# Kernel tuning notes

Hardware: AMD Instinct MI355X
Metric: run time of the kernel (lower is better)

Reference implementation:

```python
import jax, jax.numpy as jnp
import numpy as np

NUM_Q_HEADS = 16
NUM_KV_HEADS = 4
HEAD_DIM = 128
HIDDEN = NUM_Q_HEADS * HEAD_DIM
SCALE = 1.0 / HEAD_DIM ** 0.5
NUM_REP = NUM_Q_HEADS // NUM_KV_HEADS
S, B = 2048, 2


def setup_inputs() -> dict:
    key = jax.random.key(0)
    kq, kk, kv = jax.random.split(key, 3)
    query = jax.random.normal(kq, (S, B, NUM_Q_HEADS, HEAD_DIM), dtype=jnp.float32)
    k = jax.random.normal(kk, (S, B, NUM_KV_HEADS, HEAD_DIM), dtype=jnp.float32)
    v = jax.random.normal(kv, (S, B, NUM_KV_HEADS, HEAD_DIM), dtype=jnp.float32)
    return {"query": query, "key": k, "value": v}


def _attn(query, key, value):
    # GQA: repeat kv heads [S,B,Hkv,D] -> [S,B,Hq,D]
    key = jnp.repeat(key, NUM_REP, axis=2)
    value = jnp.repeat(value, NUM_REP, axis=2)
    # fp32 scores, causal mask, softmax (matches torch reference math)
    q32, k32, v32 = query.astype(jnp.float32), key.astype(jnp.float32), value.astype(jnp.float32)
    scores = jnp.einsum('sbhd,tbhd->bhst', q32, k32) * SCALE  # [B,Hq,S,S]
    s = scores.shape[-1]
    causal = jnp.tril(jnp.ones((s, s), dtype=bool))
    scores = jnp.where(causal, scores, -jnp.inf)
    attn = jax.nn.softmax(scores, axis=-1)
    out = jnp.einsum('bhst,tbhd->sbhd', attn, v32)  # [S,B,Hq,D]
    return out.astype(query.dtype).reshape(out.shape[0], out.shape[1], HIDDEN)


def reference(query, key, value) -> jnp.ndarray:
    return _attn(query, key, value)
```

## Files before the change

kernel.cpp:

```cpp
#include <hip/hip_runtime.h>
#include <cstdint>
#include <cstddef>

#define S_LEN 2048
#define BATCH 2
#define HQ    16
#define HKV   4
#define DH    128
#define KVB   64
#define QT0   64
#define KVB0  32
#define VP    40
#define PP    40

typedef float  f4     __attribute__((ext_vector_type(4)));
typedef float  f32x4  __attribute__((ext_vector_type(4)));
typedef float  f32x16 __attribute__((ext_vector_type(16)));
typedef short  short8 __attribute__((ext_vector_type(8)));
typedef unsigned u32x4 __attribute__((ext_vector_type(4)));
typedef __bf16 bf16x8 __attribute__((ext_vector_type(8)));

__device__ __forceinline__ unsigned short f2bf(float x) {
    unsigned u = __builtin_bit_cast(unsigned, x);
    u += 0x7fffu + ((u >> 16) & 1u);
    return (unsigned short)(u >> 16);
}
__device__ __forceinline__ void gld16(const void* g, void* l) {
    __builtin_amdgcn_global_load_lds(
        (const __attribute__((address_space(1))) unsigned int*)g,
        (__attribute__((address_space(3))) unsigned int*)l, 16, 0, 0);
}
__device__ __forceinline__ unsigned cvtpk_bf16(float lo, float hi) {
    unsigned r;
    asm("v_cvt_pk_bf16_f32 %0, %1, %2" : "=v"(r) : "v"(lo), "v"(hi));
    return r;
}

__global__ __launch_bounds__(256)
void prep_k(const float* __restrict__ K, short* __restrict__ out) {
    const int blk = blockIdx.x, bh = blk >> 5, tile = blk & 31, tid = threadIdx.x;
    const int r  = tid >> 2;
    const int s  = tile * 64 + r;
    const int c0 = (tid & 3) * 32;
    const float* src = K + ((size_t)s * (BATCH * HKV) + bh) * DH + c0;
    short* dst = out + ((size_t)bh * S_LEN + s) * DH;
    const int sw = (r & 7) << 3;
    #pragma unroll
    for (int ks = 0; ks < 4; ++ks) {
        f4 a  = ((const f4*)src)[ks * 2];
        f4 b2 = ((const f4*)src)[ks * 2 + 1];
        short8 o;
        #pragma unroll
        for (int j = 0; j < 4; ++j) { o[j] = (short)f2bf(a[j]); o[4 + j] = (short)f2bf(b2[j]); }
        *(short8*)&dst[(c0 + ks * 8) ^ sw] = o;
    }
}

__global__ __launch_bounds__(256)
void prep_v(const float* __restrict__ V, short* __restrict__ out) {
    __shared__ short t[64][136];
    const int blk = blockIdx.x, bh = blk >> 5, tile = blk & 31, tid = threadIdx.x;
    {
        const int r  = tid >> 2;
        const int c0 = (tid & 3) * 32;
        const float* src = V + ((size_t)(tile * 64 + r) * (BATCH * HKV) + bh) * DH + c0;
        #pragma unroll
        for (int m = 0; m < 8; ++m) {
            f4 x = ((const f4*)src)[m];
            #pragma unroll
            for (int j = 0; j < 4; ++j) t[r][c0 + m * 4 + j] = (short)f2bf(x[j]);
        }
    }
    __syncthreads();
    {
        const int d   = tid >> 1;
        const int cc0 = (tid & 1) * 32;
        const int sw  = (d & 7) << 3;
        short* dst = out + (size_t)bh * (S_LEN * DH) + (size_t)tile * (64 * DH) + d * 64 + cc0;
        #pragma unroll
        for (int c8 = 0; c8 < 4; ++c8) {
            const int base = (cc0 + c8 * 8) ^ sw;
            short8 v;
            #pragma unroll
            for (int j = 0; j < 8; ++j) v[j] = t[base + j][d];
            ((short8*)dst)[c8] = v;
        }
    }
}

__global__ __launch_bounds__(512, 1)
void fattn_main(const float* __restrict__ Q, const short* __restrict__ Kb,
                const short* __restrict__ Vb, float* __restrict__ O)
{
    __shared__ short kb[2][2][KVB * DH];
    __shared__ short vb[2][2][DH * KVB];
    __shared__ float xbuf[8][32];

    const int bh  = blockIdx.x;
    const int b   = bh >> 4, h = bh & 15, hkv = h >> 2;
    const int bh2 = b * HKV + hkv;
    const int qx  = 15 - (int)blockIdx.y;
    const int tid = threadIdx.x;
    const int wid = tid >> 6;
    const int lane = tid & 63;
    const int lq  = lane & 31;
    const int hi  = lane >> 5;
    const int half = wid >> 2;
    const int wq0  = qx * 128 + (wid & 3) * 32;
    const int nlo  = qx + 1;

    const float QS = 0.127517244f;
    bf16x8 qf[8];
    {
        const float* qp = Q + ((size_t)(wq0 + lq) * BATCH + b) * (HQ * DH) + h * DH + 8 * hi;
        #pragma unroll
        for (int dstp = 0; dstp < 8; ++dstp) {
            f4 v0 = ((const f4*)(qp + dstp * 16))[0];
            f4 v1 = ((const f4*)(qp + dstp * 16))[1];
            short8 tq;
            #pragma unroll
            for (int j = 0; j < 4; ++j) {
                tq[j]     = (short)f2bf(v0[j] * QS);
                tq[4 + j] = (short)f2bf(v1[j] * QS);
            }
            qf[dstp] = __builtin_bit_cast(bf16x8, tq);
        }
    }

    f32x16 accO[4];
    #pragma unroll
    for (int dblk = 0; dblk < 4; ++dblk)
        #pragma unroll
        for (int r = 0; r < 16; ++r) accO[dblk][r] = 0.f;
    float m = -3.0e38f, dsum = 0.f;

    const char* ksrc = (const char*)(Kb + (size_t)bh2 * S_LEN * DH);
    const char* vsrc = (const char*)(Vb + (size_t)bh2 * S_LEN * DH);

    auto stage = [&](int i) {
        const int tile = (wid >> 2) ? (nlo + i) : i;
        const int isV  = (wid >> 1) & 1;
        const char* src = (isV ? vsrc : ksrc) + (size_t)tile * 16384 + (size_t)(wid & 1) * 8192;
        char* dst = (isV ? (char*)&vb[wid >> 2][i & 1][0] : (char*)&kb[wid >> 2][i & 1][0])
                    + (wid & 1) * 8192;
        #pragma unroll
        for (int j = 0; j < 8; ++j) gld16(src + j * 1024 + lane * 16, dst + j * 1024);
    };

    stage(0);
    __syncthreads();

    for (int i = 0; i < nlo; ++i) {
        if (i + 1 < nlo) stage(i + 1);
        const int t   = half ? (nlo + i) : i;
        const int kv0 = t * 64;
        if (kv0 <= wq0 + 31) {
            const short* kc = kb[half][i & 1];
            const short* vc = vb[half][i & 1];

            f32x16 s0, s1;
            #pragma unroll
            for (int r = 0; r < 16; ++r) { s0[r] = 0.f; s1[r] = 0.f; }
            const int ksw = (lq & 7) << 3;
            const int kr0 = lq * DH, kr1 = (32 + lq) * DH;
            __builtin_amdgcn_s_setprio(1);
            #pragma unroll
            for (int dstp = 0; dstp < 8; ++dstp) {
                const int off = (dstp * 16 + 8 * hi) ^ ksw;
                short8 k0 = *(const short8*)&kc[kr0 + off];
                short8 k1 = *(const short8*)&kc[kr1 + off];
                s0 = __builtin_amdgcn_mfma_f32_32x32x16_bf16(
                    __builtin_bit_cast(bf16x8, k0), qf[dstp], s0, 0, 0, 0);
                s1 = __builtin_amdgcn_mfma_f32_32x32x16_bf16(
                    __builtin_bit_cast(bf16x8, k1), qf[dstp], s1, 0, 0, 0);
            }
            __builtin_amdgcn_s_setprio(0);

            if (kv0 + 63 > wq0) {
                const int q = wq0 + lq;
                const int kvb = kv0 + 4 * hi;
                #pragma unroll
                for (int r = 0; r < 16; ++r) {
                    const int crow = (r & 3) + 8 * (r >> 2);
                    if (kvb + crow > q)      s0[r] = -3.0e38f;
                    if (kvb + 32 + crow > q) s1[r] = -3.0e38f;
                }
            }

            float pm = fmaxf(s0[0], s1[0]);
            #pragma unroll
            for (int r = 1; r < 16; ++r) pm = fmaxf(pm, fmaxf(s0[r], s1[r]));
            pm = fmaxf(pm, __shfl_xor(pm, 32));

            if (!__all(pm <= m + 8.0f)) {
                const float mn = fmaxf(m, pm);
                const float al = __builtin_amdgcn_exp2f(m - mn);
                m = mn;
                if (lane < 32) xbuf[wid][lq] = al;
                #pragma unroll
                for (int g = 0; g < 4; ++g) {
                    f4 av = *(const f4*)&xbuf[wid][g * 8 + 4 * hi];
                    #pragma unroll
                    for (int i2 = 0; i2 < 4; ++i2) {
                        #pragma unroll
                        for (int dblk = 0; dblk < 4; ++dblk)
                            accO[dblk][g * 4 + i2] *= av[i2];
                    }
                }
                dsum *= al;
            }

            float rs = 0.f;
            #pragma unroll
            for (int r = 0; r < 16; ++r) { s0[r] = __builtin_amdgcn_exp2f(s0[r] - m); rs += s0[r]; }
            #pragma unroll
            for (int r = 0; r < 16; ++r) { s1[r] = __builtin_amdgcn_exp2f(s1[r] - m); rs += s1[r]; }
            rs += __shfl_xor(rs, 32);
            dsum += rs;

            bf16x8 pf[4];
            #pragma unroll
            for (int kst = 0; kst < 4; ++kst) {
                const int bo = (kst & 1) * 8;
                float p0, p1, p2, p3, p4, p5, p6, p7;
                if (kst < 2) {
                    p0 = s0[bo + 0]; p1 = s0[bo + 1]; p2 = s0[bo + 2]; p3 = s0[bo + 3];
                    p4 = s0[bo + 4]; p5 = s0[bo + 5]; p6 = s0[bo + 6]; p7 = s0[bo + 7];
                } else {
                    p0 = s1[bo + 0]; p1 = s1[bo + 1]; p2 = s1[bo + 2]; p3 = s1[bo + 3];
                    p4 = s1[bo + 4]; p5 = s1[bo + 5]; p6 = s1[bo + 6]; p7 = s1[bo + 7];
                }
                const unsigned c0 = cvtpk_bf16(p0, p1);
                const unsigned c1 = cvtpk_bf16(p2, p3);
                const unsigned c2 = cvtpk_bf16(p4, p5);
                const unsigned c3 = cvtpk_bf16(p6, p7);
                const unsigned sc0 = (unsigned)__shfl_xor((int)c0, 32);
                const unsigned sc1 = (unsigned)__shfl_xor((int)c1, 32);
                const unsigned sc2 = (unsigned)__shfl_xor((int)c2, 32);
                const unsigned sc3 = (unsigned)__shfl_xor((int)c3, 32);
                u32x4 pw;
                pw[0] = hi ? sc2 : c0;
                pw[1] = hi ? sc3 : c1;
                pw[2] = hi ? c2  : sc0;
                pw[3] = hi ? c3  : sc1;
                pf[kst] = __builtin_bit_cast(bf16x8, pw);
            }

            const int vsw = (lq & 7) << 3;
            __builtin_amdgcn_s_setprio(1);
            #pragma unroll
            for (int kst = 0; kst < 4; ++kst) {
                const int voff = kst * 16 + 8 * hi;
                #pragma unroll
                for (int dblk = 0; dblk < 4; ++dblk) {
                    const int d = dblk * 32 + lq;
                    short8 vv = *(const short8*)&vc[d * KVB + (voff ^ vsw)];
                    accO[dblk] = __builtin_amdgcn_mfma_f32_32x32x16_bf16(
                        pf[kst], __builtin_bit_cast(bf16x8, vv), accO[dblk], 0, 0, 0);
                }
            }
            __builtin_amdgcn_s_setprio(0);
        }
        __syncthreads();
    }

    if (lane < 32) xbuf[wid][lq] = m;
    __syncthreads();
    const float mo = xbuf[wid ^ 4][lq];
    const float ms = fmaxf(m, mo);
    const float aa = __builtin_amdgcn_exp2f(m - ms);
    dsum *= aa;
    __syncthreads();
    if (lane < 32) xbuf[wid][lq] = dsum;
    __syncthreads();
    dsum += xbuf[wid ^ 4][lq];
    __syncthreads();
    if (lane < 32) xbuf[wid][lq] = aa;
    #pragma unroll
    for (int g = 0; g < 4; ++g) {
        f4 av = *(const f4*)&xbuf[wid][g * 8 + 4 * hi];
        #pragma unroll
        for (int i2 = 0; i2 < 4; ++i2) {
            #pragma unroll
            for (int dblk = 0; dblk < 4; ++dblk)
                accO[dblk][g * 4 + i2] *= av[i2];
        }
    }
    __syncthreads();
    float* mb = (float*)&kb[0][0][0];
    if (half) {
        float* slot = mb + (size_t)(wid & 3) * 4096;
        #pragma unroll
        for (int dblk = 0; dblk < 4; ++dblk)
            #pragma unroll
            for (int r2 = 0; r2 < 4; ++r2) {
                f4 v;
                #pragma unroll
                for (int j = 0; j < 4; ++j) v[j] = accO[dblk][r2 * 4 + j];
                *(f4*)&slot[(dblk * 4 + r2) * 256 + lane * 4] = v;
            }
    }
    __syncthreads();
    if (!half) {
        float* slot = mb + (size_t)(wid & 3) * 4096;
        #pragma unroll
        for (int dblk = 0; dblk < 4; ++dblk)
            #pragma unroll
            for (int r2 = 0; r2 < 4; ++r2) {
                f4 v = *(const f4*)&slot[(dblk * 4 + r2) * 256 + lane * 4];
                #pragma unroll
                for (int j = 0; j < 4; ++j) accO[dblk][r2 * 4 + j] += v[j];
            }
        if (lane < 32) xbuf[wid][lq] = dsum;
        #pragma unroll
        for (int g = 0; g < 4; ++g) {
            f4 dv = *(const f4*)&xbuf[wid][g * 8 + 4 * hi];
            #pragma unroll
            for (int i2 = 0; i2 < 4; ++i2) {
                const float inv = 1.0f / dv[i2];
                const int row = wq0 + g * 8 + i2 + 4 * hi;
                float* op = O + ((size_t)row * BATCH + b) * (HQ * DH) + h * DH + lq;
                #pragma unroll
                for (int dblk = 0; dblk < 4; ++dblk)
                    op[dblk * 32] = accO[dblk][g * 4 + i2] * inv;
            }
        }
    }
}

__global__ __launch_bounds__(256)
void fattn_fallback(const float* __restrict__ Q, const float* __restrict__ K,
                    const float* __restrict__ V, float* __restrict__ O)
{
    __shared__ short kbuf[KVB0 * DH];
    __shared__ short vbuf[DH * VP];
    __shared__ short pbuf[4][16 * PP];

    const int bh  = blockIdx.y;
    const int b   = bh >> 4, h = bh & 15, hkv = h >> 2;
    const int q0  = blockIdx.x * QT0;
    const int tid = threadIdx.x;
    const int wid = tid >> 6;
    const int lane = tid & 63;
    const int lr  = lane & 15;
    const int kb2 = lane >> 4;
    const int qr  = q0 + wid * 16;

    const float QS = 0.127517244f;
    bf16x8 qf[4];
    {
        const float* qp = Q + ((size_t)(qr + lr) * BATCH + b) * (HQ * DH) + h * DH + kb2 * 8;
        #pragma unroll
        for (int ks = 0; ks < 4; ++ks) {
            f4 v0 = ((const f4*)(qp + ks * 32))[0];
            f4 v1 = ((const f4*)(qp + ks * 32))[1];
            short8 tq;
            #pragma unroll
            for (int j = 0; j < 4; ++j) {
                tq[j]     = (short)f2bf(v0[j] * QS);
                tq[4 + j] = (short)f2bf(v1[j] * QS);
            }
            qf[ks] = __builtin_bit_cast(bf16x8, tq);
        }
    }

    float mr[4], ls[4];
    f32x4 accO[8];
    #pragma unroll
    for (int r = 0; r < 4; ++r) { mr[r] = -3.0e38f; ls[r] = 0.0f; }
    #pragma unroll
    for (int d = 0; d < 8; ++d) accO[d] = (f32x4){0.f, 0.f, 0.f, 0.f};

    const int sr  = tid >> 3, sc = tid & 7;
    const int vr2 = (tid >> 4) * 2, vc8 = tid & 15;
    const int ntiles = q0 / KVB0 + 2;

    for (int t = 0; t < ntiles; ++t) {
        const int kv0 = t * KVB0;
        {
            const float* kp = K + ((size_t)(kv0 + sr) * BATCH + b) * (HKV * DH) + hkv * DH + sc * 16;
            f4 a0 = ((const f4*)kp)[0];
            f4 a1 = ((const f4*)kp)[1];
            f4 a2 = ((const f4*)kp)[2];
            f4 a3 = ((const f4*)kp)[3];
            short8 s0v, s1v;
            #pragma unroll
            for (int j = 0; j < 4; ++j) {
                s0v[j] = (short)f2bf(a0[j]); s0v[4 + j] = (short)f2bf(a1[j]);
                s1v[j] = (short)f2bf(a2[j]); s1v[4 + j] = (short)f2bf(a3[j]);
            }
            const int sw = (sr & 7) << 3;
            *(short8*)&kbuf[sr * DH + ((sc * 16) ^ sw)]     = s0v;
            *(short8*)&kbuf[sr * DH + ((sc * 16 + 8) ^ sw)] = s1v;
        }
        {
            const float* vp0 = V + ((size_t)(kv0 + vr2) * BATCH + b) * (HKV * DH) + hkv * DH + vc8 * 8;
            const float* vp1 = vp0 + (size_t)BATCH * HKV * DH;
            f4 b0 = ((const f4*)vp0)[0];
            f4 b1 = ((const f4*)vp0)[1];
            f4 c0 = ((const f4*)vp1)[0];
            f4 c1 = ((const f4*)vp1)[1];
            float va[8]  = {b0[0], b0[1], b0[2], b0[3], b1[0], b1[1], b1[2], b1[3]};
            float vbv[8] = {c0[0], c0[1], c0[2], c0[3], c1[0], c1[1], c1[2], c1[3]};
            #pragma unroll
            for (int j = 0; j < 8; ++j) {
                const int d = vc8 * 8 + j;
                unsigned pk = (unsigned)f2bf(va[j]) | ((unsigned)f2bf(vbv[j]) << 16);
                const int rsw = (((vr2 >> 3) ^ ((d >> 3) & 3)) << 3) + (vr2 & 7);
                *(unsigned*)&vbuf[d * VP + rsw] = pk;
            }
        }
        __syncthreads();

        f32x4 sf[2];
        sf[0] = (f32x4){0.f, 0.f, 0.f, 0.f};
        sf[1] = (f32x4){0.f, 0.f, 0.f, 0.f};
        #pragma unroll
        for (int cb = 0; cb < 2; ++cb) {
            const int krow = cb * 16 + lr;
            const int sw = (krow & 7) << 3;
            #pragma unroll
            for (int ks = 0; ks < 4; ++ks) {
                short8 kkf = *(const short8*)&kbuf[krow * DH + ((ks * 32 + kb2 * 8) ^ sw)];
                sf[cb] = __builtin_amdgcn_mfma_f32_16x16x32_bf16(
                    qf[ks], __builtin_bit_cast(bf16x8, kkf), sf[cb], 0, 0, 0);
            }
        }
        if (kv0 + KVB0 - 1 > qr) {
            #pragma unroll
            for (int cb = 0; cb < 2; ++cb) {
                const int col = kv0 + cb * 16 + lr;
                #pragma unroll
                for (int r = 0; r < 4; ++r)
                    if (col > qr + kb2 * 4 + r) sf[cb][r] = -3.0e38f;
            }
        }
        float al[4];
        #pragma unroll
        for (int r = 0; r < 4; ++r) {
            float rm = fmaxf(sf[0][r], sf[1][r]);
            rm = fmaxf(rm, __shfl_xor(rm, 1));
            rm = fmaxf(rm, __shfl_xor(rm, 2));
            rm = fmaxf(rm, __shfl_xor(rm, 4));
            rm = fmaxf(rm, __shfl_xor(rm, 8));
            const float mn = fmaxf(mr[r], rm);
            al[r] = exp2f(mr[r] - mn);
            mr[r] = mn;
            const unsigned short pk0 = f2bf(exp2f(sf[0][r] - mn));
            const unsigned short pk1 = f2bf(exp2f(sf[1][r] - mn));
            pbuf[wid][(kb2 * 4 + r) * PP + lr]      = (short)pk0;
            pbuf[wid][(kb2 * 4 + r) * PP + 16 + lr] = (short)pk1;
            float ps = __builtin_bit_cast(float, (unsigned)pk0 << 16)
                     + __builtin_bit_cast(float, (unsigned)pk1 << 16);
            ps += __shfl_xor(ps, 1);
            ps += __shfl_xor(ps, 2);
            ps += __shfl_xor(ps, 4);
            ps += __shfl_xor(ps, 8);
            ls[r] = ls[r] * al[r] + ps;
        }
        #pragma unroll
        for (int d = 0; d < 8; ++d) {
            #pragma unroll
            for (int r = 0; r < 4; ++r) accO[d][r] *= al[r];
        }
        const short8 pA = *(const short8*)&pbuf[wid][lr * PP + kb2 * 8];
        #pragma unroll
        for (int db = 0; db < 8; ++db) {
            const int d = db * 16 + lr;
            const int rc = ((kb2 ^ ((d >> 3) & 3)) << 3);
            short8 vv = *(const short8*)&vbuf[d * VP + rc];
            accO[db] = __builtin_amdgcn_mfma_f32_16x16x32_bf16(
                __builtin_bit_cast(bf16x8, pA), __builtin_bit_cast(bf16x8, vv), accO[db], 0, 0, 0);
        }
        __syncthreads();
    }

    #pragma unroll
    for (int r = 0; r < 4; ++r) ls[r] = 1.0f / ls[r];
    #pragma unroll
    for (int db = 0; db < 8; ++db) {
        #pragma unroll
        for (int r = 0; r < 4; ++r) {
            const int row = qr + kb2 * 4 + r;
            O[((size_t)row * BATCH + b) * (HQ * DH) + h * DH + db * 16 + lr] = accO[db][r] * ls[r];
        }
    }
}

extern "C" void kernel_launch(void* const* d_in, const int* in_sizes, int n_in,
                              void* d_out, int out_size, void* d_ws, size_t ws_size,
                              hipStream_t stream)
{
    (void)in_sizes; (void)n_in; (void)out_size;
    const float* Q = (const float*)d_in[0];
    const float* K = (const float*)d_in[1];
    const float* V = (const float*)d_in[2];
    float* O = (float*)d_out;

    const size_t kv_elems = (size_t)BATCH * HKV * S_LEN * DH;
    const size_t need = kv_elems * 2 * sizeof(short);
    if (ws_size >= need) {
        short* Kb = (short*)d_ws;
        short* Vb = Kb + kv_elems;
        prep_k<<<dim3(BATCH * HKV * (S_LEN / 64)), dim3(256), 0, stream>>>(K, Kb);
        prep_v<<<dim3(BATCH * HKV * (S_LEN / 64)), dim3(256), 0, stream>>>(V, Vb);
        dim3 grid(BATCH * HQ, 16);
        fattn_main<<<grid, dim3(512), 0, stream>>>(Q, Kb, Vb, O);
    } else {
        dim3 grid(S_LEN / QT0, BATCH * HQ);
        fattn_fallback<<<grid, dim3(256), 0, stream>>>(Q, K, V, O);
    }
}
```

Before: 74.88 us.

## Split causal KV loop across four wave groups with 32-wide tiles

fattn_main grows from 8 to 16 waves per block. Four query-row groups each walk an interleaved stream of 32-wide KV tiles instead of two halves walking 64-wide tiles. Each step then runs half the MFMAs per wave, with its own masking and softmax. prep_v is rewritten to emit the V layout these 32-column tiles need. A multi-stage LDS reduction merges the four partial softmax states and outputs, which adds more barriers and a launch-bounds setting that may constrain registers.

```diff
diff --git a/kernel.cpp b/kernel.cpp
--- a/kernel.cpp
+++ b/kernel.cpp
@@ -7,7 +7,6 @@
 #define HQ    16
 #define HKV   4
 #define DH    128
-#define KVB   64
 #define QT0   64
 #define KVB0  32
 #define VP    40
@@ -59,11 +58,11 @@
 __global__ __launch_bounds__(256)
 void prep_v(const float* __restrict__ V, short* __restrict__ out) {
     __shared__ short t[64][136];
-    const int blk = blockIdx.x, bh = blk >> 5, tile = blk & 31, tid = threadIdx.x;
+    const int blk = blockIdx.x, bh = blk >> 5, tile64 = blk & 31, tid = threadIdx.x;
     {
         const int r  = tid >> 2;
         const int c0 = (tid & 3) * 32;
-        const float* src = V + ((size_t)(tile * 64 + r) * (BATCH * HKV) + bh) * DH + c0;
+        const float* src = V + ((size_t)(tile64 * 64 + r) * (BATCH * HKV) + bh) * DH + c0;
         #pragma unroll
         for (int m = 0; m < 8; ++m) {
             f4 x = ((const f4*)src)[m];
@@ -74,27 +73,32 @@
     __syncthreads();
     {
         const int d   = tid >> 1;
-        const int cc0 = (tid & 1) * 32;
-        const int sw  = (d & 7) << 3;
-        short* dst = out + (size_t)bh * (S_LEN * DH) + (size_t)tile * (64 * DH) + d * 64 + cc0;
-        #pragma unroll
-        for (int c8 = 0; c8 < 4; ++c8) {
-            const int base = (cc0 + c8 * 8) ^ sw;
-            short8 v;
-            #pragma unroll
-            for (int j = 0; j < 8; ++j) v[j] = t[base + j][d];
-            ((short8*)dst)[c8] = v;
-        }
-    }
-}
-
-__global__ __launch_bounds__(512, 1)
+        const int h16 = tid & 1;
+        const int rr  = d >> 1;
+        const int sw  = (rr & 7) << 3;
+        short* base = out + (size_t)bh * (S_LEN * DH);
+        #pragma unroll
+        for (int a = 0; a < 2; ++a) {
+            short* dst = base + (size_t)(2 * tile64 + a) * 4096 + rr * 64;
+            #pragma unroll
+            for (int g = 0; g < 2; ++g) {
+                const int kv0 = h16 * 16 + g * 8;
+                const int cb  = (d & 1) * 32 + kv0;
+                short8 v;
+                #pragma unroll
+                for (int j = 0; j < 8; ++j) v[j] = t[a * 32 + kv0 + j][d];
+                *(short8*)&dst[cb ^ sw] = v;
+            }
+        }
+    }
+}
+
+__global__ __launch_bounds__(1024, 4)
 void fattn_main(const float* __restrict__ Q, const short* __restrict__ Kb,
                 const short* __restrict__ Vb, float* __restrict__ O)
 {
-    __shared__ short kb[2][2][KVB * DH];
-    __shared__ short vb[2][2][DH * KVB];
-    __shared__ float xbuf[8][32];
+    __shared__ short kvs[4][2][2][4096];
+    __shared__ float xbuf[16][32];
 
     const int bh  = blockIdx.x;
     const int b   = bh >> 4, h = bh & 15, hkv = h >> 2;
@@ -105,9 +109,10 @@
     const int lane = tid & 63;
     const int lq  = lane & 31;
     const int hi  = lane >> 5;
-    const int half = wid >> 2;
-    const int wq0  = qx * 128 + (wid & 3) * 32;
-    const int nlo  = qx + 1;
+    const int rw  = wid & 3;
+    const int qt  = wid >> 2;
+    const int wq0 = qx * 128 + rw * 32;
+    const int nit = qx + 1;
 
     const float QS = 0.127517244f;
     bf16x8 qf[8];
@@ -138,58 +143,51 @@
     const char* vsrc = (const char*)(Vb + (size_t)bh2 * S_LEN * DH);
 
     auto stage = [&](int i) {
-        const int tile = (wid >> 2) ? (nlo + i) : i;
-        const int isV  = (wid >> 1) & 1;
-        const char* src = (isV ? vsrc : ksrc) + (size_t)tile * 16384 + (size_t)(wid & 1) * 8192;
-        char* dst = (isV ? (char*)&vb[wid >> 2][i & 1][0] : (char*)&kb[wid >> 2][i & 1][0])
-                    + (wid & 1) * 8192;
-        #pragma unroll
-        for (int j = 0; j < 8; ++j) gld16(src + j * 1024 + lane * 16, dst + j * 1024);
+        const int qs  = wid >> 2;
+        const int isV = (wid >> 1) & 1;
+        const int t   = 4 * i + qs;
+        const char* src = (isV ? vsrc : ksrc) + (size_t)t * 8192 + (size_t)(wid & 1) * 4096;
+        char* dst = (char*)&kvs[qs][i & 1][isV][0] + (wid & 1) * 4096;
+        #pragma unroll
+        for (int j = 0; j < 4; ++j) gld16(src + j * 1024 + lane * 16, dst + j * 1024);
     };
 
     stage(0);
     __syncthreads();
 
-    for (int i = 0; i < nlo; ++i) {
-        if (i + 1 < nlo) stage(i + 1);
-        const int t   = half ? (nlo + i) : i;
-        const int kv0 = t * 64;
+    for (int i = 0; i < nit; ++i) {
+        if (i + 1 < nit) stage(i + 1);
+        const int kv0 = (4 * i + qt) * 32;
         if (kv0 <= wq0 + 31) {
-            const short* kc = kb[half][i & 1];
-            const short* vc = vb[half][i & 1];
-
-            f32x16 s0, s1;
-            #pragma unroll
-            for (int r = 0; r < 16; ++r) { s0[r] = 0.f; s1[r] = 0.f; }
+            const short* kc = &kvs[qt][i & 1][0][0];
+            const short* vc = &kvs[qt][i & 1][1][0];
+
+            f32x16 s0;
+            #pragma unroll
+            for (int r = 0; r < 16; ++r) s0[r] = 0.f;
             const int ksw = (lq & 7) << 3;
-            const int kr0 = lq * DH, kr1 = (32 + lq) * DH;
             __builtin_amdgcn_s_setprio(1);
             #pragma unroll
             for (int dstp = 0; dstp < 8; ++dstp) {
-                const int off = (dstp * 16 + 8 * hi) ^ ksw;
-                short8 k0 = *(const short8*)&kc[kr0 + off];
-                short8 k1 = *(const short8*)&kc[kr1 + off];
+                short8 k0 = *(const short8*)&kc[lq * DH + ((dstp * 16 + 8 * hi) ^ ksw)];
                 s0 = __builtin_amdgcn_mfma_f32_32x32x16_bf16(
                     __builtin_bit_cast(bf16x8, k0), qf[dstp], s0, 0, 0, 0);
-                s1 = __builtin_amdgcn_mfma_f32_32x32x16_bf16(
-                    __builtin_bit_cast(bf16x8, k1), qf[dstp], s1, 0, 0, 0);
             }
             __builtin_amdgcn_s_setprio(0);
 
-            if (kv0 + 63 > wq0) {
+            if (kv0 + 31 > wq0) {
                 const int q = wq0 + lq;
                 const int kvb = kv0 + 4 * hi;
                 #pragma unroll
                 for (int r = 0; r < 16; ++r) {
                     const int crow = (r & 3) + 8 * (r >> 2);
-                    if (kvb + crow > q)      s0[r] = -3.0e38f;
-                    if (kvb + 32 + crow > q) s1[r] = -3.0e38f;
+                    if (kvb + crow > q) s0[r] = -3.0e38f;
                 }
             }
 
-            float pm = fmaxf(s0[0], s1[0]);
-            #pragma unroll
-            for (int r = 1; r < 16; ++r) pm = fmaxf(pm, fmaxf(s0[r], s1[r]));
+            float pm = s0[0];
+            #pragma unroll
+            for (int r = 1; r < 16; ++r) pm = fmaxf(pm, s0[r]);
             pm = fmaxf(pm, __shfl_xor(pm, 32));
 
             if (!__all(pm <= m + 8.0f)) {
@@ -213,27 +211,17 @@
             float rs = 0.f;
             #pragma unroll
             for (int r = 0; r < 16; ++r) { s0[r] = __builtin_amdgcn_exp2f(s0[r] - m); rs += s0[r]; }
-            #pragma unroll
-            for (int r = 0; r < 16; ++r) { s1[r] = __builtin_amdgcn_exp2f(s1[r] - m); rs += s1[r]; }
             rs += __shfl_xor(rs, 32);
             dsum += rs;
 
-            bf16x8 pf[4];
-            #pragma unroll
-            for (int kst = 0; kst < 4; ++kst) {
-                const int bo = (kst & 1) * 8;
-                float p0, p1, p2, p3, p4, p5, p6, p7;
-                if (kst < 2) {
-                    p0 = s0[bo + 0]; p1 = s0[bo + 1]; p2 = s0[bo + 2]; p3 = s0[bo + 3];
-                    p4 = s0[bo + 4]; p5 = s0[bo + 5]; p6 = s0[bo + 6]; p7 = s0[bo + 7];
-                } else {
-                    p0 = s1[bo + 0]; p1 = s1[bo + 1]; p2 = s1[bo + 2]; p3 = s1[bo + 3];
-                    p4 = s1[bo + 4]; p5 = s1[bo + 5]; p6 = s1[bo + 6]; p7 = s1[bo + 7];
-                }
-                const unsigned c0 = cvtpk_bf16(p0, p1);
-                const unsigned c1 = cvtpk_bf16(p2, p3);
-                const unsigned c2 = cvtpk_bf16(p4, p5);
-                const unsigned c3 = cvtpk_bf16(p6, p7);
+            bf16x8 pf[2];
+            #pragma unroll
+            for (int kst = 0; kst < 2; ++kst) {
+                const int bo = kst * 8;
+                const unsigned c0 = cvtpk_bf16(s0[bo + 0], s0[bo + 1]);
+                const unsigned c1 = cvtpk_bf16(s0[bo + 2], s0[bo + 3]);
+                const unsigned c2 = cvtpk_bf16(s0[bo + 4], s0[bo + 5]);
+                const unsigned c3 = cvtpk_bf16(s0[bo + 6], s0[bo + 7]);
                 const unsigned sc0 = (unsigned)__shfl_xor((int)c0, 32);
                 const unsigned sc1 = (unsigned)__shfl_xor((int)c1, 32);
                 const unsigned sc2 = (unsigned)__shfl_xor((int)c2, 32);
@@ -246,15 +234,15 @@
                 pf[kst] = __builtin_bit_cast(bf16x8, pw);
             }
 
-            const int vsw = (lq & 7) << 3;
             __builtin_amdgcn_s_setprio(1);
             #pragma unroll
-            for (int kst = 0; kst < 4; ++kst) {
-                const int voff = kst * 16 + 8 * hi;
+            for (int kst = 0; kst < 2; ++kst) {
                 #pragma unroll
                 for (int dblk = 0; dblk < 4; ++dblk) {
-                    const int d = dblk * 32 + lq;
-                    short8 vv = *(const short8*)&vc[d * KVB + (voff ^ vsw)];
+                    const int d  = dblk * 32 + lq;
+                    const int rr = d >> 1;
+                    const int col = (d & 1) * 32 + kst * 16 + 8 * hi;
+                    short8 vv = *(const short8*)&vc[rr * 64 + (col ^ ((rr & 7) << 3))];
                     accO[dblk] = __builtin_amdgcn_mfma_f32_32x32x16_bf16(
                         pf[kst], __builtin_bit_cast(bf16x8, vv), accO[dblk], 0, 0, 0);
                 }
@@ -266,14 +254,14 @@
 
     if (lane < 32) xbuf[wid][lq] = m;
     __syncthreads();
-    const float mo = xbuf[wid ^ 4][lq];
-    const float ms = fmaxf(m, mo);
-    const float aa = __builtin_amdgcn_exp2f(m - ms);
+    const float m4 = fmaxf(fmaxf(xbuf[rw][lq], xbuf[rw + 4][lq]),
+                           fmaxf(xbuf[rw + 8][lq], xbuf[rw + 12][lq]));
+    const float aa = __builtin_amdgcn_exp2f(m - m4);
     dsum *= aa;
     __syncthreads();
     if (lane < 32) xbuf[wid][lq] = dsum;
     __syncthreads();
-    dsum += xbuf[wid ^ 4][lq];
+    const float dtot = xbuf[rw][lq] + xbuf[rw + 4][lq] + xbuf[rw + 8][lq] + xbuf[rw + 12][lq];
     __syncthreads();
     if (lane < 32) xbuf[wid][lq] = aa;
     #pragma unroll
@@ -287,9 +275,9 @@
         }
     }
     __syncthreads();
-    float* mb = (float*)&kb[0][0][0];
-    if (half) {
-        float* slot = mb + (size_t)(wid & 3) * 4096;
+    float* mb = (float*)&kvs[0][0][0][0];
+    if (qt == 1 || qt == 3) {
+        float* slot = mb + (size_t)(rw + ((qt == 3) ? 4 : 0)) * 4096;
         #pragma unroll
         for (int dblk = 0; dblk < 4; ++dblk)
             #pragma unroll
@@ -301,8 +289,8 @@
             }
     }
     __syncthreads();
-    if (!half) {
-        float* slot = mb + (size_t)(wid & 3) * 4096;
+    if (qt == 0 || qt == 2) {
+        float* slot = mb + (size_t)(rw + ((qt == 2) ? 4 : 0)) * 4096;
         #pragma unroll
         for (int dblk = 0; dblk < 4; ++dblk)
             #pragma unroll
@@ -311,7 +299,33 @@
                 #pragma unroll
                 for (int j = 0; j < 4; ++j) accO[dblk][r2 * 4 + j] += v[j];
             }
-        if (lane < 32) xbuf[wid][lq] = dsum;
+    }
+    __syncthreads();
+    if (qt == 2) {
+        float* slot = mb + (size_t)rw * 4096;
+        #pragma unroll
+        for (int dblk = 0; dblk < 4; ++dblk)
+            #pragma unroll
+            for (int r2 = 0; r2 < 4; ++r2) {
+                f4 v;
+                #pragma unroll
+                for (int j = 0; j < 4; ++j) v[j] = accO[dblk][r2 * 4 + j];
+                *(f4*)&slot[(dblk * 4 + r2) * 256 + lane * 4] = v;
+            }
+    }
+    __syncthreads();
+    if (lane < 32) xbuf[wid][lq] = dtot;
+    __syncthreads();
+    if (qt == 0) {
+        float* slot = mb + (size_t)rw * 4096;
+        #pragma unroll
+        for (int dblk = 0; dblk < 4; ++dblk)
+            #pragma unroll
+            for (int r2 = 0; r2 < 4; ++r2) {
+                f4 v = *(const f4*)&slot[(dblk * 4 + r2) * 256 + lane * 4];
+                #pragma unroll
+                for (int j = 0; j < 4; ++j) accO[dblk][r2 * 4 + j] += v[j];
+            }
         #pragma unroll
         for (int g = 0; g < 4; ++g) {
             f4 dv = *(const f4*)&xbuf[wid][g * 8 + 4 * hi];
@@ -505,7 +519,7 @@
         prep_k<<<dim3(BATCH * HKV * (S_LEN / 64)), dim3(256), 0, stream>>>(K, Kb);
         prep_v<<<dim3(BATCH * HKV * (S_LEN / 64)), dim3(256), 0, stream>>>(V, Vb);
         dim3 grid(BATCH * HQ, 16);
-        fattn_main<<<grid, dim3(512), 0, stream>>>(Q, Kb, Vb, O);
+        fattn_main<<<grid, dim3(1024), 0, stream>>>(Q, Kb, Vb, O);
     } else {
         dim3 grid(S_LEN / QT0, BATCH * HQ);
         fattn_fallback<<<grid, dim3(256), 0, stream>>>(Q, K, V, O);
```

Measured after the change: 139.5 us. 1.86x slower.

## Split KV halves into separate workgroups and merge partial outputs in a second kernel

Applied to the files above, without the earlier changes.

Replaces the single 512-thread block that processes two KV halves internally with 256-thread blocks, one per KV half, doubling the grid and allowing two blocks per CU. Each block writes an unnormalized partial output plus its row max and sum to workspace. A new merge kernel combines the two halves with log-sum-exp rescaling. The aim is better occupancy and load balance, at the cost of an extra fp32 output round trip through global memory and another kernel launch. The old kernel is kept as a fallback when the workspace is too small.

```diff
diff --git a/kernel.cpp b/kernel.cpp
--- a/kernel.cpp
+++ b/kernel.cpp
@@ -88,26 +88,28 @@
     }
 }
 
-__global__ __launch_bounds__(512, 1)
-void fattn_main(const float* __restrict__ Q, const short* __restrict__ Kb,
-                const short* __restrict__ Vb, float* __restrict__ O)
+__global__ __launch_bounds__(256, 2)
+void fattn_half(const float* __restrict__ Q, const short* __restrict__ Kb,
+                const short* __restrict__ Vb, float* __restrict__ Olo,
+                float* __restrict__ Whi, float* __restrict__ ml)
 {
-    __shared__ short kb[2][2][KVB * DH];
-    __shared__ short vb[2][2][DH * KVB];
-    __shared__ float xbuf[8][32];
+    __shared__ short kb[2][KVB * DH];
+    __shared__ short vb[2][DH * KVB];
+    __shared__ float xbuf[4][32];
 
     const int bh  = blockIdx.x;
     const int b   = bh >> 4, h = bh & 15, hkv = h >> 2;
     const int bh2 = b * HKV + hkv;
-    const int qx  = 15 - (int)blockIdx.y;
+    const int y   = blockIdx.y;
+    const int qx  = 15 - (y >> 1);
+    const int half = y & 1;
     const int tid = threadIdx.x;
     const int wid = tid >> 6;
     const int lane = tid & 63;
     const int lq  = lane & 31;
     const int hi  = lane >> 5;
-    const int half = wid >> 2;
-    const int wq0  = qx * 128 + (wid & 3) * 32;
-    const int nlo  = qx + 1;
+    const int wq0 = qx * 128 + wid * 32;
+    const int nlo = qx + 1;
 
     const float QS = 0.127517244f;
     bf16x8 qf[8];
@@ -138,11 +140,10 @@
     const char* vsrc = (const char*)(Vb + (size_t)bh2 * S_LEN * DH);
 
     auto stage = [&](int i) {
-        const int tile = (wid >> 2) ? (nlo + i) : i;
-        const int isV  = (wid >> 1) & 1;
-        const char* src = (isV ? vsrc : ksrc) + (size_t)tile * 16384 + (size_t)(wid & 1) * 8192;
-        char* dst = (isV ? (char*)&vb[wid >> 2][i & 1][0] : (char*)&kb[wid >> 2][i & 1][0])
-                    + (wid & 1) * 8192;
+        const int t   = half ? (nlo + i) : i;
+        const int isV = (wid >> 1) & 1;
+        const char* src = (isV ? vsrc : ksrc) + (size_t)t * 16384 + (size_t)(wid & 1) * 8192;
+        char* dst = (isV ? (char*)&vb[i & 1][0] : (char*)&kb[i & 1][0]) + (wid & 1) * 8192;
         #pragma unroll
         for (int j = 0; j < 8; ++j) gld16(src + j * 1024 + lane * 16, dst + j * 1024);
     };
@@ -155,8 +156,8 @@
         const int t   = half ? (nlo + i) : i;
         const int kv0 = t * 64;
         if (kv0 <= wq0 + 31) {
-            const short* kc = kb[half][i & 1];
-            const short* vc = vb[half][i & 1];
+            const short* kc = kb[i & 1];
+            const short* vc = vb[i & 1];
 
             f32x16 s0, s1;
             #pragma unroll
@@ -264,6 +265,229 @@
         __syncthreads();
     }
 
+    const int part = (qx * 32 + bh) * 2 + half;
+    if (lane < 32) {
+        ml[(size_t)part * 256 + wid * 32 + lq]       = m;
+        ml[(size_t)part * 256 + 128 + wid * 32 + lq] = dsum;
+    }
+    float* Od = half ? Whi : Olo;
+    #pragma unroll
+    for (int g = 0; g < 4; ++g) {
+        #pragma unroll
+        for (int i2 = 0; i2 < 4; ++i2) {
+            const int row = wq0 + g * 8 + i2 + 4 * hi;
+            float* op = Od + ((size_t)row * BATCH + b) * (HQ * DH) + h * DH + lq;
+            #pragma unroll
+            for (int dblk = 0; dblk < 4; ++dblk)
+                op[dblk * 32] = accO[dblk][g * 4 + i2];
+        }
+    }
+}
+
+__global__ __launch_bounds__(256)
+void merge_halves(float* __restrict__ O, const float* __restrict__ Whi,
+                  const float* __restrict__ ml)
+{
+    const int bh = blockIdx.x;
+    const int qx = blockIdx.y;
+    const int b = bh >> 4, h = bh & 15;
+    const int tid = threadIdx.x;
+    const int part0 = (qx * 32 + bh) * 2;
+    const int part1 = part0 + 1;
+    const int d  = tid & 127;
+    const int rh = tid >> 7;
+    for (int r2 = 0; r2 < 64; ++r2) {
+        const int qq  = r2 * 2 + rh;
+        const int row = qx * 128 + qq;
+        const float ma = ml[(size_t)part0 * 256 + qq];
+        const float da = ml[(size_t)part0 * 256 + 128 + qq];
+        const float mb = ml[(size_t)part1 * 256 + qq];
+        const float db = ml[(size_t)part1 * 256 + 128 + qq];
+        const float ms = fmaxf(ma, mb);
+        const float ea = __builtin_amdgcn_exp2f(ma - ms);
+        const float eb = __builtin_amdgcn_exp2f(mb - ms);
+        const float inv = 1.0f / (da * ea + db * eb);
+        const size_t off = ((size_t)row * BATCH + b) * (HQ * DH) + h * DH + d;
+        O[off] = (O[off] * ea + Whi[off] * eb) * inv;
+    }
+}
+
+__global__ __launch_bounds__(512, 1)
+void fattn_main_r11(const float* __restrict__ Q, const short* __restrict__ Kb,
+                    const short* __restrict__ Vb, float* __restrict__ O)
+{
+    __shared__ short kb[2][2][KVB * DH];
+    __shared__ short vb[2][2][DH * KVB];
+    __shared__ float xbuf[8][32];
+
+    const int bh  = blockIdx.x;
+    const int b   = bh >> 4, h = bh & 15, hkv = h >> 2;
+    const int bh2 = b * HKV + hkv;
+    const int qx  = 15 - (int)blockIdx.y;
+    const int tid = threadIdx.x;
+    const int wid = tid >> 6;
+    const int lane = tid & 63;
+    const int lq  = lane & 31;
+    const int hi  = lane >> 5;
+    const int half = wid >> 2;
+    const int wq0  = qx * 128 + (wid & 3) * 32;
+    const int nlo  = qx + 1;
+
+    const float QS = 0.127517244f;
+    bf16x8 qf[8];
+    {
+        const float* qp = Q + ((size_t)(wq0 + lq) * BATCH + b) * (HQ * DH) + h * DH + 8 * hi;
+        #pragma unroll
+        for (int dstp = 0; dstp < 8; ++dstp) {
+            f4 v0 = ((const f4*)(qp + dstp * 16))[0];
+            f4 v1 = ((const f4*)(qp + dstp * 16))[1];
+            short8 tq;
+            #pragma unroll
+            for (int j = 0; j < 4; ++j) {
+                tq[j]     = (short)f2bf(v0[j] * QS);
+                tq[4 + j] = (short)f2bf(v1[j] * QS);
+            }
+            qf[dstp] = __builtin_bit_cast(bf16x8, tq);
+        }
+    }
+
+    f32x16 accO[4];
+    #pragma unroll
+    for (int dblk = 0; dblk < 4; ++dblk)
+        #pragma unroll
+        for (int r = 0; r < 16; ++r) accO[dblk][r] = 0.f;
+    float m = -3.0e38f, dsum = 0.f;
+
+    const char* ksrc = (const char*)(Kb + (size_t)bh2 * S_LEN * DH);
+    const char* vsrc = (const char*)(Vb + (size_t)bh2 * S_LEN * DH);
+
+    auto stage = [&](int i) {
+        const int tile = (wid >> 2) ? (nlo + i) : i;
+        const int isV  = (wid >> 1) & 1;
+        const char* src = (isV ? vsrc : ksrc) + (size_t)tile * 16384 + (size_t)(wid & 1) * 8192;
+        char* dst = (isV ? (char*)&vb[wid >> 2][i & 1][0] : (char*)&kb[wid >> 2][i & 1][0])
+                    + (wid & 1) * 8192;
+        #pragma unroll
+        for (int j = 0; j < 8; ++j) gld16(src + j * 1024 + lane * 16, dst + j * 1024);
+    };
+
+    stage(0);
+    __syncthreads();
+
+    for (int i = 0; i < nlo; ++i) {
+        if (i + 1 < nlo) stage(i + 1);
+        const int t   = half ? (nlo + i) : i;
+        const int kv0 = t * 64;
+        if (kv0 <= wq0 + 31) {
+            const short* kc = kb[half][i & 1];
+            const short* vc = vb[half][i & 1];
+
+            f32x16 s0, s1;
+            #pragma unroll
+            for (int r = 0; r < 16; ++r) { s0[r] = 0.f; s1[r] = 0.f; }
+            const int ksw = (lq & 7) << 3;
+            const int kr0 = lq * DH, kr1 = (32 + lq) * DH;
+            __builtin_amdgcn_s_setprio(1);
+            #pragma unroll
+            for (int dstp = 0; dstp < 8; ++dstp) {
+                const int off = (dstp * 16 + 8 * hi) ^ ksw;
+                short8 k0 = *(const short8*)&kc[kr0 + off];
+                short8 k1 = *(const short8*)&kc[kr1 + off];
+                s0 = __builtin_amdgcn_mfma_f32_32x32x16_bf16(
+                    __builtin_bit_cast(bf16x8, k0), qf[dstp], s0, 0, 0, 0);
+                s1 = __builtin_amdgcn_mfma_f32_32x32x16_bf16(
+                    __builtin_bit_cast(bf16x8, k1), qf[dstp], s1, 0, 0, 0);
+            }
+            __builtin_amdgcn_s_setprio(0);
+
+            if (kv0 + 63 > wq0) {
+                const int q = wq0 + lq;
+                const int kvb = kv0 + 4 * hi;
+                #pragma unroll
+                for (int r = 0; r < 16; ++r) {
+                    const int crow = (r & 3) + 8 * (r >> 2);
+                    if (kvb + crow > q)      s0[r] = -3.0e38f;
+                    if (kvb + 32 + crow > q) s1[r] = -3.0e38f;
+                }
+            }
+
+            float pm = fmaxf(s0[0], s1[0]);
+            #pragma unroll
+            for (int r = 1; r < 16; ++r) pm = fmaxf(pm, fmaxf(s0[r], s1[r]));
+            pm = fmaxf(pm, __shfl_xor(pm, 32));
+
+            if (!__all(pm <= m + 8.0f)) {
+                const float mn = fmaxf(m, pm);
+                const float al = __builtin_amdgcn_exp2f(m - mn);
+                m = mn;
+                if (lane < 32) xbuf[wid][lq] = al;
+                #pragma unroll
+                for (int g = 0; g < 4; ++g) {
+                    f4 av = *(const f4*)&xbuf[wid][g * 8 + 4 * hi];
+                    #pragma unroll
+                    for (int i2 = 0; i2 < 4; ++i2) {
+                        #pragma unroll
+                        for (int dblk = 0; dblk < 4; ++dblk)
+                            accO[dblk][g * 4 + i2] *= av[i2];
+                    }
+                }
+                dsum *= al;
+            }
+
+            float rs = 0.f;
+            #pragma unroll
+            for (int r = 0; r < 16; ++r) { s0[r] = __builtin_amdgcn_exp2f(s0[r] - m); rs += s0[r]; }
+            #pragma unroll
+            for (int r = 0; r < 16; ++r) { s1[r] = __builtin_amdgcn_exp2f(s1[r] - m); rs += s1[r]; }
+            rs += __shfl_xor(rs, 32);
+            dsum += rs;
+
+            bf16x8 pf[4];
+            #pragma unroll
+            for (int kst = 0; kst < 4; ++kst) {
+                const int bo = (kst & 1) * 8;
+                float p0, p1, p2, p3, p4, p5, p6, p7;
+                if (kst < 2) {
+                    p0 = s0[bo + 0]; p1 = s0[bo + 1]; p2 = s0[bo + 2]; p3 = s0[bo + 3];
+                    p4 = s0[bo + 4]; p5 = s0[bo + 5]; p6 = s0[bo + 6]; p7 = s0[bo + 7];
+                } else {
+                    p0 = s1[bo + 0]; p1 = s1[bo + 1]; p2 = s1[bo + 2]; p3 = s1[bo + 3];
+                    p4 = s1[bo + 4]; p5 = s1[bo + 5]; p6 = s1[bo + 6]; p7 = s1[bo + 7];
+                }
+                const unsigned c0 = cvtpk_bf16(p0, p1);
+                const unsigned c1 = cvtpk_bf16(p2, p3);
+                const unsigned c2 = cvtpk_bf16(p4, p5);
+                const unsigned c3 = cvtpk_bf16(p6, p7);
+                const unsigned sc0 = (unsigned)__shfl_xor((int)c0, 32);
+                const unsigned sc1 = (unsigned)__shfl_xor((int)c1, 32);
+                const unsigned sc2 = (unsigned)__shfl_xor((int)c2, 32);
+                const unsigned sc3 = (unsigned)__shfl_xor((int)c3, 32);
+                u32x4 pw;
+                pw[0] = hi ? sc2 : c0;
+                pw[1] = hi ? sc3 : c1;
+                pw[2] = hi ? c2  : sc0;
+                pw[3] = hi ? c3  : sc1;
+                pf[kst] = __builtin_bit_cast(bf16x8, pw);
+            }
+
+            const int vsw = (lq & 7) << 3;
+            __builtin_amdgcn_s_setprio(1);
+            #pragma unroll
+            for (int kst = 0; kst < 4; ++kst) {
+                const int voff = kst * 16 + 8 * hi;
+                #pragma unroll
+                for (int dblk = 0; dblk < 4; ++dblk) {
+                    const int d = dblk * 32 + lq;
+                    short8 vv = *(const short8*)&vc[d * KVB + (voff ^ vsw)];
+                    accO[dblk] = __builtin_amdgcn_mfma_f32_32x32x16_bf16(
+                        pf[kst], __builtin_bit_cast(bf16x8, vv), accO[dblk], 0, 0, 0);
+                }
+            }
+            __builtin_amdgcn_s_setprio(0);
+        }
+        __syncthreads();
+    }
+
     if (lane < 32) xbuf[wid][lq] = m;
     __syncthreads();
     const float mo = xbuf[wid ^ 4][lq];
@@ -498,14 +722,23 @@
     float* O = (float*)d_out;
 
     const size_t kv_elems = (size_t)BATCH * HKV * S_LEN * DH;
-    const size_t need = kv_elems * 2 * sizeof(short);
-    if (ws_size >= need) {
+    const size_t kv_bytes = kv_elems * 2 * sizeof(short);
+    const size_t o_elems  = (size_t)S_LEN * BATCH * HQ * DH;
+    const size_t need2    = kv_bytes + o_elems * 4 + 1024 * 256 * 4;
+
+    if (ws_size >= kv_bytes) {
         short* Kb = (short*)d_ws;
         short* Vb = Kb + kv_elems;
         prep_k<<<dim3(BATCH * HKV * (S_LEN / 64)), dim3(256), 0, stream>>>(K, Kb);
         prep_v<<<dim3(BATCH * HKV * (S_LEN / 64)), dim3(256), 0, stream>>>(V, Vb);
-        dim3 grid(BATCH * HQ, 16);
-        fattn_main<<<grid, dim3(512), 0, stream>>>(Q, Kb, Vb, O);
+        if (ws_size >= need2) {
+            float* Whi = (float*)((char*)d_ws + kv_bytes);
+            float* ml  = Whi + o_elems;
+            fattn_half<<<dim3(BATCH * HQ, 32), dim3(256), 0, stream>>>(Q, Kb, Vb, O, Whi, ml);
+            merge_halves<<<dim3(BATCH * HQ, 16), dim3(256), 0, stream>>>(O, Whi, ml);
+        } else {
+            fattn_main_r11<<<dim3(BATCH * HQ, 16), dim3(512), 0, stream>>>(Q, Kb, Vb, O);
+        }
     } else {
         dim3 grid(S_LEN / QT0, BATCH * HQ);
         fattn_fallback<<<grid, dim3(256), 0, stream>>>(Q, K, V, O);
```

Result: slower. 98.69 us (+31.8%).
